# Optimization experiments

Measured on AMD Instinct MI355X. Metric: run time of the kernel, lower is better.

The kernel has to match this reference:

```python
import jax, jax.numpy as jnp
import numpy as np

B, N, C = 8192, 64, 256  # batch, num_nodes, cells; depth=2


def setup_inputs() -> dict:
    key = jax.random.key(0)
    ks = jax.random.split(key, 9)
    scale1 = 1.0  # fan_in = 1
    scaleC = 1.0 / np.sqrt(C)
    return {
        "Q": jax.random.normal(ks[0], (B, N), dtype=jnp.float32),
        "Y": jax.random.normal(ks[1], (B, N), dtype=jnp.float32),
        # stacked per-node MLP params: Linear(1,C) -> ReLU -> Linear(C,C) -> ReLU -> Linear(C,1)
        "W1": jax.random.normal(ks[2], (N, 1, C), dtype=jnp.float32) * scale1,
        "b1": jax.random.normal(ks[3], (N, C), dtype=jnp.float32) * scale1,
        "W2": jax.random.normal(ks[4], (N, C, C), dtype=jnp.float32) * scaleC,
        "b2": jax.random.normal(ks[5], (N, C), dtype=jnp.float32) * scaleC,
        "W3": jax.random.normal(ks[6], (N, C, 1), dtype=jnp.float32) * scaleC,
        "b3": jax.random.normal(ks[7], (N, 1), dtype=jnp.float32) * scaleC,
        "bias_0": jnp.ones((1, 1), dtype=jnp.float32),
    }


def reference(Q, Y, W1, b1, W2, b2, W3, b3, bias_0):
    s = Q * Y  # [B, N], per-node scalar input s_i = q_i * y_i
    # layer 1: scalar -> C  (W1[n,0,:] broadcast over batch)
    h = jax.nn.relu(s[:, :, None] * W1[None, :, 0, :] + b1[None])  # [B, N, C]
    # layer 2: C -> C, batched over nodes
    h = jax.nn.relu(jnp.einsum("bnc,ncd->bnd", h, W2) + b2[None])  # [B, N, C]
    # layer 3: C -> scalar
    z_i = jnp.einsum("bnc,nc->bn", h, W3[:, :, 0]) + b3[None, :, 0]  # [B, N]
    z_0 = bias_0 - jnp.sum(s, axis=-1, keepdims=True)  # [B, 1]
    z = jnp.concatenate([z_0, z_i], axis=-1)  # [B, N+1]
    z = jax.nn.softmax(z, axis=-1)
    return jax.nn.relu(z)
```

## Files before the change

kernel.cpp:

```cpp
#include <hip/hip_runtime.h>
#include <hip/hip_bf16.h>


typedef unsigned int u32;
typedef __fp16 fp16x2 __attribute__((ext_vector_type(2)));
union U32H { u32 u; fp16x2 h; };

__device__ __forceinline__ u32 pkh(float a, float b) {
    U32H cv; cv.h = __builtin_amdgcn_cvt_pkrtz(a, b); return cv.u;
}
__device__ __forceinline__ float dot2f(u32 a, u32 b, float c) {
    float d;
    asm("v_dot2_f32_f16 %0, %1, %2, %3" : "=v"(d) : "v"(a), "v"(b), "v"(c));
    return d;
}

__global__ __launch_bounds__(256) void prep(
    const float* __restrict__ Q, const float* __restrict__ Y,
    const float* __restrict__ W1, const float* __restrict__ b1,
    float* __restrict__ S, float* __restrict__ knots, int* __restrict__ perm)
{
    __shared__ float ts[64][65];
    __shared__ float key[256];
    __shared__ int   idx[256];

    const int blk = blockIdx.x;
    const int tid = threadIdx.x;

    if (blk < 128) {
        const int b0 = blk << 6;
        #pragma unroll
        for (int jj = 0; jj < 16; jj++) {
            int i = tid + (jj << 8);
            int r = i >> 6, c = i & 63;
            ts[r][c] = Q[(size_t)(b0 + r) * 64 + c] * Y[(size_t)(b0 + r) * 64 + c];
        }
        __syncthreads();
        #pragma unroll
        for (int jj = 0; jj < 16; jj++) {
            int i = tid + (jj << 8);
            int nn = i >> 6, bb = i & 63;
            S[((size_t)nn << 13) + b0 + bb] = ts[bb][nn];
        }
    } else {
        const int n = blk - 128;
        {
            float w = W1[n * 256 + tid];
            float b = b1[n * 256 + tid];
            key[tid] = -b / w;
            idx[tid] = tid;
        }
        __syncthreads();
        for (int k = 2; k <= 256; k <<= 1) {
            for (int j = k >> 1; j > 0; j >>= 1) {
                int p = tid ^ j;
                if (p > tid) {
                    float a = key[tid], c = key[p];
                    bool up = ((tid & k) == 0);
                    if (up ? (a > c) : (a < c)) {
                        int ia = idx[tid];
                        key[tid] = c; idx[tid] = idx[p];
                        key[p] = a; idx[p] = ia;
                    }
                }
                __syncthreads();
            }
        }
        knots[n * 256 + tid] = key[tid];
        perm[n * 256 + tid]  = idx[tid];
    }
}

__global__ __launch_bounds__(256) void build_sort(
    const float* __restrict__ W1, const float* __restrict__ b1,
    const float* __restrict__ W2, const float* __restrict__ b2,
    const int* __restrict__ perm, const float* __restrict__ S,
    const float* __restrict__ knots,
    uint2* __restrict__ table, uint2* __restrict__ sorted)
{
    __shared__ float w1s[256], b1s[256];
    __shared__ int   pm[256];
    __shared__ float part[16][16][8];
    __shared__ u32   hist[257];

    const int blk = blockIdx.x;
    const int tid = threadIdx.x;
    const int lane = tid & 63;

    if (blk < 512) {
        const int n    = blk >> 3;
        const int strip= blk & 7;
        const int prl  = tid & 15;
        const int seg  = tid >> 4;
        const int prg  = (strip << 4) + prl;
        const int d0   = prg << 1;

        w1s[tid] = W1[n * 256 + tid];
        b1s[tid] = b1[n * 256 + tid];
        pm[tid]  = perm[n * 256 + tid];
        __syncthreads();

        const float* W2n = W2 + ((size_t)n << 16);

        {
            float ba0 = 0.f, bc0 = 0.f, ba1 = 0.f, bc1 = 0.f;
            float da0 = 0.f, dc0 = 0.f, da1 = 0.f, dc1 = 0.f;
            #pragma unroll 4
            for (int i = 0; i < 16; ++i) {
                int   kj = pm[(seg << 4) + i];
                float w  = w1s[kj];
                float bb = b1s[kj];
                float2 v = *reinterpret_cast<const float2*>(&W2n[kj * 256 + d0]);
                if (w < 0.f) {
                    ba0 = fmaf(v.x, w, ba0); bc0 = fmaf(v.x, bb, bc0);
                    ba1 = fmaf(v.y, w, ba1); bc1 = fmaf(v.y, bb, bc1);
                }
                float aw = fabsf(w);
                float cs = (w > 0.f) ? bb : -bb;
                da0 = fmaf(v.x, aw, da0); dc0 = fmaf(v.x, cs, dc0);
                da1 = fmaf(v.y, aw, da1); dc1 = fmaf(v.y, cs, dc1);
            }
            float* p = part[seg][prl];
            p[0] = ba0; p[1] = bc0; p[2] = ba1; p[3] = bc1;
            p[4] = da0; p[5] = dc0; p[6] = da1; p[7] = dc1;
        }
        __syncthreads();

        if (tid < 16) {
            const int pr = tid;
            float sa0 = 0.f, sc0 = 0.f, sa1 = 0.f, sc1 = 0.f;
            #pragma unroll
            for (int sg = 0; sg < 16; ++sg) {
                const float* p = part[sg][pr];
                sa0 += p[0]; sc0 += p[1]; sa1 += p[2]; sc1 += p[3];
            }
            const int dd = ((strip << 4) + pr) << 1;
            sc0 += b2[n * 256 + dd];
            sc1 += b2[n * 256 + dd + 1];
            table[(size_t)n * 257 * 128 + ((strip << 4) + pr)] =
                make_uint2(pkh(sa0, sa1), pkh(sc0, sc1));
            float ra0 = sa0, rc0 = sc0, ra1 = sa1, rc1 = sc1;
            #pragma unroll
            for (int sg = 0; sg < 16; ++sg) {
                float* p = part[sg][pr];
                float t4 = p[4], t5 = p[5], t6 = p[6], t7 = p[7];
                p[0] = ra0; p[1] = rc0; p[2] = ra1; p[3] = rc1;
                ra0 += t4; rc0 += t5; ra1 += t6; rc1 += t7;
            }
        }
        __syncthreads();

        {
            const float* p = part[seg][prl];
            float a0 = p[0], c0 = p[1], a1 = p[2], c1 = p[3];
            uint2* trow = table + (size_t)n * 257 * 128 + prg;
            #pragma unroll 4
            for (int i = 0; i < 16; ++i) {
                int   j  = (seg << 4) + i;
                int   kj = pm[j];
                float w  = w1s[kj];
                float bb = b1s[kj];
                float2 v = *reinterpret_cast<const float2*>(&W2n[kj * 256 + d0]);
                float aw = fabsf(w);
                float cs = (w > 0.f) ? bb : -bb;
                a0 = fmaf(v.x, aw, a0); c0 = fmaf(v.x, cs, c0);
                a1 = fmaf(v.y, aw, a1); c1 = fmaf(v.y, cs, c1);
                trow[(size_t)(j + 1) * 128] = make_uint2(pkh(a0, a1), pkh(c0, c1));
            }
        }
    } else {
        const int t = blk - 512;
        const int n = t >> 2;
        const int q = t & 3;

        float* kn = w1s;
        kn[tid] = knots[n * 256 + tid];
        hist[tid] = 0;
        if (tid == 0) hist[256] = 0;
        __syncthreads();

        const float* Sn = S + ((size_t)n << 13) + (q << 11);
        float sv[8]; int iv[8];
        #pragma unroll
        for (int j = 0; j < 8; ++j) {
            const float s = Sn[tid + (j << 8)];
            sv[j] = s;
            int I = 0;
            #pragma unroll
            for (int step = 128; step >= 1; step >>= 1)
                if (kn[I + step - 1] < s) I += step;
            if (I < 256 && kn[I] < s) I += 1;
            iv[j] = I;
            atomicAdd(&hist[I], 1u);
        }
        __syncthreads();

        if (tid < 64) {
            int base = tid << 2;
            u32 h0 = hist[base], h1 = hist[base + 1], h2 = hist[base + 2], h3 = hist[base + 3];
            u32 lsum = h0 + h1 + h2 + h3;
            u32 run = lsum;
            #pragma unroll
            for (int off = 1; off < 64; off <<= 1) {
                u32 tt = __shfl_up(run, off, 64);
                if (lane >= off) run += tt;
            }
            u32 excl = run - lsum;
            hist[base]     = excl;
            hist[base + 1] = excl + h0;
            hist[base + 2] = excl + h0 + h1;
            hist[base + 3] = excl + h0 + h1 + h2;
            if (tid == 63) hist[256] = excl + lsum;
        }
        __syncthreads();

        uint2* dst = sorted + ((size_t)n << 13) + (q << 11);
        #pragma unroll
        for (int j = 0; j < 8; ++j) {
            u32 pos = atomicAdd(&hist[iv[j]], 1u);
            u32 bglob = (u32)((q << 11) + tid + (j << 8));
            dst[pos] = make_uint2(__float_as_uint(sv[j]), ((u32)iv[j] << 13) | bglob);
        }
    }
}

__global__ __launch_bounds__(256) void eval_nodes(
    const uint2* __restrict__ sorted, const uint2* __restrict__ table,
    const float* __restrict__ W3, const float* __restrict__ b3,
    float* __restrict__ Z)
{
    __shared__ u32 w3p[128];

    const int n   = blockIdx.x;
    const int c0  = blockIdx.y << 8;
    const int tid = threadIdx.x;

    if (tid < 128)
        w3p[tid] = pkh(W3[n * 256 + (tid << 1)], W3[n * 256 + (tid << 1) + 1]);
    __syncthreads();

    const uint2 ent = sorted[((size_t)n << 13) + c0 + tid];
    const float s   = __uint_as_float(ent.x);
    const int   I   = (int)(ent.y >> 13);
    const int   bl  = (int)(ent.y & 8191u);

    U32H s2; s2.u = pkh(s, s);
    const fp16x2 z2 = (fp16x2)0;

    const uint4* row = reinterpret_cast<const uint4*>(
        table + (size_t)((u32)n * 257 + I) * 128);

    float acc0 = 0.f, acc1 = 0.f;
    #pragma unroll 4
    for (int q = 0; q < 64; ++q) {
        uint4 v = row[q];
        uint2 w = reinterpret_cast<const uint2*>(w3p)[q];
        U32H a01{v.x}, b01{v.y}, a23{v.z}, b23{v.w};
        U32H h01, h23;
        h01.h = __builtin_elementwise_max(a01.h * s2.h + b01.h, z2);
        h23.h = __builtin_elementwise_max(a23.h * s2.h + b23.h, z2);
        acc0 = dot2f(h01.u, w.x, acc0);
        acc1 = dot2f(h23.u, w.y, acc1);
    }
    Z[((size_t)n << 13) + bl] = acc0 + acc1 + b3[n];
}

__global__ __launch_bounds__(256) void softmax_rows(
    const float* __restrict__ Q, const float* __restrict__ Y,
    const float* __restrict__ Z, const float* __restrict__ bias0,
    float* __restrict__ out)
{
    __shared__ float ts[64][65];
    const int b0   = blockIdx.x << 6;
    const int tid  = threadIdx.x;
    const int lane = tid & 63;
    const int wv   = tid >> 6;

    #pragma unroll
    for (int jj = 0; jj < 16; jj++) {
        int idx = tid + (jj << 8);
        int nn = idx >> 6, bb = idx & 63;
        ts[bb][nn] = Z[((size_t)nn << 13) + b0 + bb];
    }
    __syncthreads();

    const float bias = bias0[0];
    #pragma unroll 2
    for (int r = 0; r < 16; ++r) {
        const int row = (wv << 4) + r;
        const int b   = b0 + row;

        float s = Q[(size_t)b * 64 + lane] * Y[(size_t)b * 64 + lane];
        float ssum = s;
        #pragma unroll
        for (int mask = 32; mask >= 1; mask >>= 1) ssum += __shfl_xor(ssum, mask, 64);
        const float z0 = bias - ssum;

        float zl = ts[row][lane];
        float mx = zl;
        #pragma unroll
        for (int mask = 32; mask >= 1; mask >>= 1) mx = fmaxf(mx, __shfl_xor(mx, mask, 64));
        mx = fmaxf(mx, z0);

        float el = expf(zl - mx);
        float e0 = expf(z0 - mx);
        float den = el;
        #pragma unroll
        for (int mask = 32; mask >= 1; mask >>= 1) den += __shfl_xor(den, mask, 64);
        den += e0;
        const float inv = 1.0f / den;

        out[(size_t)b * 65 + 1 + lane] = el * inv;
        if (lane == 0) out[(size_t)b * 65] = e0 * inv;
    }
}

extern "C" void kernel_launch(void* const* d_in, const int* in_sizes, int n_in,
                              void* d_out, int out_size, void* d_ws, size_t ws_size,
                              hipStream_t stream)
{
    const float* Q     = (const float*)d_in[0];
    const float* Y     = (const float*)d_in[1];
    const float* W1    = (const float*)d_in[2];
    const float* b1    = (const float*)d_in[3];
    const float* W2    = (const float*)d_in[4];
    const float* b2    = (const float*)d_in[5];
    const float* W3    = (const float*)d_in[6];
    const float* b3    = (const float*)d_in[7];
    const float* bias0 = (const float*)d_in[8];
    float* out = (float*)d_out;

    char* ws = (char*)d_ws;
    uint2* table  = (uint2*)ws;
    float* S      = (float*)(ws + 16842752);
    float* Z      = (float*)(ws + 18939904);
    float* knots  = (float*)(ws + 21037056);
    int*   perm   = (int*)  (ws + 21102592);
    uint2* sorted = (uint2*)(ws + 21168128);

    prep<<<192, 256, 0, stream>>>(Q, Y, W1, b1, S, knots, perm);
    build_sort<<<768, 256, 0, stream>>>(W1, b1, W2, b2, perm, S, knots, table, sorted);
    eval_nodes<<<dim3(64, 32), 256, 0, stream>>>(sorted, table, W3, b3, Z);
    softmax_rows<<<128, 256, 0, stream>>>(Q, Y, Z, bias0, out);
}
```

Measured before the change: 63.61 us.

## Process two sorted samples per thread in eval_nodes and cache W2 loads in registers

eval_nodes now gives each thread two adjacent sorted entries, loaded together as one uint4. When both fall in the same knot interval, the table row is read once and reused for both. The grid is halved to match. In build_sort, the W2 values loaded in the first pass are kept in a fully unrolled register array so the second pass does not reload them from global memory. The trade-off is higher register pressure and fewer threads in eval_nodes, plus a divergent branch when neighbouring entries fall in different intervals.

```diff
diff --git a/kernel.cpp b/kernel.cpp
--- a/kernel.cpp
+++ b/kernel.cpp
@@ -101,16 +101,18 @@
         __syncthreads();
 
         const float* W2n = W2 + ((size_t)n << 16);
+        float2 vreg[16];
 
         {
             float ba0 = 0.f, bc0 = 0.f, ba1 = 0.f, bc1 = 0.f;
             float da0 = 0.f, dc0 = 0.f, da1 = 0.f, dc1 = 0.f;
-            #pragma unroll 4
+            #pragma unroll
             for (int i = 0; i < 16; ++i) {
                 int   kj = pm[(seg << 4) + i];
                 float w  = w1s[kj];
                 float bb = b1s[kj];
                 float2 v = *reinterpret_cast<const float2*>(&W2n[kj * 256 + d0]);
+                vreg[i] = v;
                 if (w < 0.f) {
                     ba0 = fmaf(v.x, w, ba0); bc0 = fmaf(v.x, bb, bc0);
                     ba1 = fmaf(v.y, w, ba1); bc1 = fmaf(v.y, bb, bc1);
@@ -154,13 +156,13 @@
             const float* p = part[seg][prl];
             float a0 = p[0], c0 = p[1], a1 = p[2], c1 = p[3];
             uint2* trow = table + (size_t)n * 257 * 128 + prg;
-            #pragma unroll 4
+            #pragma unroll
             for (int i = 0; i < 16; ++i) {
                 int   j  = (seg << 4) + i;
                 int   kj = pm[j];
                 float w  = w1s[kj];
                 float bb = b1s[kj];
-                float2 v = *reinterpret_cast<const float2*>(&W2n[kj * 256 + d0]);
+                float2 v = vreg[i];
                 float aw = fabsf(w);
                 float cs = (w > 0.f) ? bb : -bb;
                 a0 = fmaf(v.x, aw, a0); c0 = fmaf(v.x, cs, c0);
@@ -232,37 +234,71 @@
     __shared__ u32 w3p[128];
 
     const int n   = blockIdx.x;
-    const int c0  = blockIdx.y << 8;
+    const int c0  = blockIdx.y << 9;
     const int tid = threadIdx.x;
 
     if (tid < 128)
         w3p[tid] = pkh(W3[n * 256 + (tid << 1)], W3[n * 256 + (tid << 1) + 1]);
     __syncthreads();
 
-    const uint2 ent = sorted[((size_t)n << 13) + c0 + tid];
-    const float s   = __uint_as_float(ent.x);
-    const int   I   = (int)(ent.y >> 13);
-    const int   bl  = (int)(ent.y & 8191u);
-
-    U32H s2; s2.u = pkh(s, s);
+    const uint4 ee = *reinterpret_cast<const uint4*>(
+        sorted + ((size_t)n << 13) + c0 + (tid << 1));
+    const float s0 = __uint_as_float(ee.x);
+    const int   I0 = (int)(ee.y >> 13);
+    const int   o0 = (int)(ee.y & 8191u);
+    const float s1 = __uint_as_float(ee.z);
+    const int   I1 = (int)(ee.w >> 13);
+    const int   o1 = (int)(ee.w & 8191u);
+
+    U32H sa; sa.u = pkh(s0, s0);
+    U32H sb; sb.u = pkh(s1, s1);
     const fp16x2 z2 = (fp16x2)0;
-
-    const uint4* row = reinterpret_cast<const uint4*>(
-        table + (size_t)((u32)n * 257 + I) * 128);
-
-    float acc0 = 0.f, acc1 = 0.f;
-    #pragma unroll 4
-    for (int q = 0; q < 64; ++q) {
-        uint4 v = row[q];
-        uint2 w = reinterpret_cast<const uint2*>(w3p)[q];
-        U32H a01{v.x}, b01{v.y}, a23{v.z}, b23{v.w};
-        U32H h01, h23;
-        h01.h = __builtin_elementwise_max(a01.h * s2.h + b01.h, z2);
-        h23.h = __builtin_elementwise_max(a23.h * s2.h + b23.h, z2);
-        acc0 = dot2f(h01.u, w.x, acc0);
-        acc1 = dot2f(h23.u, w.y, acc1);
-    }
-    Z[((size_t)n << 13) + bl] = acc0 + acc1 + b3[n];
+    const float b3n = b3[n];
+
+    const uint4* row0 = reinterpret_cast<const uint4*>(
+        table + (size_t)((u32)n * 257 + I0) * 128);
+
+    float a00 = 0.f, a01 = 0.f, a10 = 0.f, a11 = 0.f;
+    if (I0 == I1) {
+        #pragma unroll 4
+        for (int q = 0; q < 64; ++q) {
+            uint4 v = row0[q];
+            uint2 w = reinterpret_cast<const uint2*>(w3p)[q];
+            U32H p01{v.x}, q01{v.y}, p23{v.z}, q23{v.w};
+            U32H h;
+            h.h = __builtin_elementwise_max(p01.h * sa.h + q01.h, z2);
+            a00 = dot2f(h.u, w.x, a00);
+            h.h = __builtin_elementwise_max(p23.h * sa.h + q23.h, z2);
+            a01 = dot2f(h.u, w.y, a01);
+            h.h = __builtin_elementwise_max(p01.h * sb.h + q01.h, z2);
+            a10 = dot2f(h.u, w.x, a10);
+            h.h = __builtin_elementwise_max(p23.h * sb.h + q23.h, z2);
+            a11 = dot2f(h.u, w.y, a11);
+        }
+    } else {
+        const uint4* row1 = reinterpret_cast<const uint4*>(
+            table + (size_t)((u32)n * 257 + I1) * 128);
+        #pragma unroll 2
+        for (int q = 0; q < 64; ++q) {
+            uint4 v0 = row0[q];
+            uint4 v1 = row1[q];
+            uint2 w = reinterpret_cast<const uint2*>(w3p)[q];
+            U32H h;
+            { U32H p01{v0.x}, q01{v0.y}, p23{v0.z}, q23{v0.w};
+              h.h = __builtin_elementwise_max(p01.h * sa.h + q01.h, z2);
+              a00 = dot2f(h.u, w.x, a00);
+              h.h = __builtin_elementwise_max(p23.h * sa.h + q23.h, z2);
+              a01 = dot2f(h.u, w.y, a01); }
+            { U32H p01{v1.x}, q01{v1.y}, p23{v1.z}, q23{v1.w};
+              h.h = __builtin_elementwise_max(p01.h * sb.h + q01.h, z2);
+              a10 = dot2f(h.u, w.x, a10);
+              h.h = __builtin_elementwise_max(p23.h * sb.h + q23.h, z2);
+              a11 = dot2f(h.u, w.y, a11); }
+        }
+    }
+    float* Zn = Z + ((size_t)n << 13);
+    Zn[o0] = a00 + a01 + b3n;
+    Zn[o1] = a10 + a11 + b3n;
 }
 
 __global__ __launch_bounds__(256) void softmax_rows(
@@ -340,6 +376,6 @@
 
     prep<<<192, 256, 0, stream>>>(Q, Y, W1, b1, S, knots, perm);
     build_sort<<<768, 256, 0, stream>>>(W1, b1, W2, b2, perm, S, knots, table, sorted);
-    eval_nodes<<<dim3(64, 32), 256, 0, stream>>>(sorted, table, W3, b3, Z);
+    eval_nodes<<<dim3(64, 16), 256, 0, stream>>>(sorted, table, W3, b3, Z);
     softmax_rows<<<128, 256, 0, stream>>>(Q, Y, Z, bias0, out);
 }
```

After: 72.57 us. +14.1%, slower.
